# Kernel tuning notes

Hardware: AMD Instinct MI355X
Metric: run time of the kernel (lower is better)

Reference implementation:

```python
import jax, jax.numpy as jnp
import numpy as np

IN_CH = 128
OUT_CH = 32
HEADS = 4
N_NODES = 50000
N_EDGES = 500000
NEG_SLOPE = 0.01  # torch leaky_relu default


def setup_inputs() -> dict:
    key = jax.random.key(0)
    ks = jax.random.split(key, 8)
    E, D, H, C = N_EDGES, IN_CH, HEADS, OUT_CH
    receivers = jax.random.normal(ks[0], (E, D), dtype=jnp.float32)
    senders = jax.random.normal(ks[1], (E, D), dtype=jnp.float32)
    edge_attribute = jax.random.normal(ks[2], (E, D), dtype=jnp.float32)
    sender_idx = jax.random.randint(ks[3], (E,), 0, N_NODES)
    receiver_idx = jax.random.randint(ks[4], (E,), 0, N_NODES)
    # bias-free linear weights, stored as [in, heads*out] so y = x @ W
    scale = 1.0 / np.sqrt(D)
    W_src = jax.random.normal(ks[5], (D, H * C), dtype=jnp.float32) * scale
    W_tgt = jax.random.normal(ks[6], (D, H * C), dtype=jnp.float32) * scale
    W_edge = jax.random.normal(ks[7], (D, H * C), dtype=jnp.float32) * scale
    # xavier_normal_ on shape (1, H, C): std = sqrt(2/(H + C)) per torch fan calc on last two dims
    attn = jax.random.normal(jax.random.fold_in(key, 99), (1, H, C), dtype=jnp.float32) * np.sqrt(2.0 / (H + C))
    return {
        "receivers": receivers,
        "senders": senders,
        "edge_attribute": edge_attribute,
        "sender_idx": sender_idx,
        "receiver_idx": receiver_idx,
        "W_src": W_src,
        "W_tgt": W_tgt,
        "W_edge": W_edge,
        "attn": attn,
    }


def reference(receivers, senders, edge_attribute, sender_idx, receiver_idx, W_src, W_tgt, W_edge, attn):
    E = receivers.shape[0]
    H, C = HEADS, OUT_CH
    t = (receivers @ W_tgt).reshape(E, H, C)   # target projection of receiver feats
    s = (senders @ W_src).reshape(E, H, C)
    e = (edge_attribute @ W_edge).reshape(E, H, C)
    z = (jax.nn.leaky_relu(s + t + e, NEG_SLOPE) * attn).sum(-1)  # [E, H]
    # segment softmax over edges grouped by sender_idx
    zmax = jax.ops.segment_max(z, sender_idx, num_segments=N_NODES)  # [N, H]
    ez = jnp.exp(z - zmax[sender_idx])
    denom = jax.ops.segment_sum(ez, sender_idx, num_segments=N_NODES)
    a = ez / denom[sender_idx]                 # [E, H]
    m = t * a[..., None]                        # [E, H, C]
    aggr_m = jax.ops.segment_sum(m, receiver_idx, num_segments=N_NODES)  # [N, H, C]
    return aggr_m.mean(axis=1), m.mean(axis=1)  # ([N, C], [E, C])
```

## Files before the change

### kernel.cpp

```cpp
#include <hip/hip_runtime.h>
#include <hip/hip_bf16.h>

#define E_EDGES 500000
#define NN 50000

typedef unsigned short u16;
typedef __attribute__((ext_vector_type(8))) short s16x8;
typedef __attribute__((ext_vector_type(4))) float f32x4;

#define BAR() __builtin_amdgcn_s_barrier()
#define SCHED0() __builtin_amdgcn_sched_barrier(0)
#define WAITLGKM0() asm volatile("s_waitcnt lgkmcnt(0)" ::: "memory")

__device__ __forceinline__ short f2bf(float f) {
    unsigned u = __builtin_bit_cast(unsigned, f);
    u += 0x7fffu + ((u >> 16) & 1u);
    return (short)(u >> 16);
}

__device__ __forceinline__ float lrelu(float x) { return x > 0.0f ? x : 0.01f * x; }

__device__ __forceinline__ s16x8 cvt8(float4 lo, float4 hi) {
    union { s16x8 v; __hip_bfloat162 h[4]; } u;
    u.h[0] = __float22bfloat162_rn(make_float2(lo.x, lo.y));
    u.h[1] = __float22bfloat162_rn(make_float2(lo.z, lo.w));
    u.h[2] = __float22bfloat162_rn(make_float2(hi.x, hi.y));
    u.h[3] = __float22bfloat162_rn(make_float2(hi.z, hi.w));
    return u.v;
}

__global__ void kprep(const float* __restrict__ Wsrc, const float* __restrict__ Wtgt,
                      const float* __restrict__ Wedge, u16* __restrict__ WT) {
    int i = blockIdx.x * 256 + threadIdx.x;
    if (i >= 3 * 16384) return;
    int g = i >> 14, nk = i & 16383, n = nk >> 7, k = nk & 127;
    const float* W = (g == 0) ? Wsrc : (g == 1) ? Wtgt : Wedge;
    WT[i] = (u16)f2bf(W[k * 128 + n]);
}

__global__ __launch_bounds__(256, 2) void k1(
    const float* __restrict__ recv, const float* __restrict__ send,
    const float* __restrict__ eattr, const int* __restrict__ sidx,
    const u16* __restrict__ WT, const float* __restrict__ attn,
    float* __restrict__ ez, float* __restrict__ denom)
{
    __shared__ u16 ldsA[128][136];
    __shared__ u16 ldsB[128][136];
    __shared__ float smEz[4][32][4];
    const int tid = threadIdx.x;
    const int lane = tid & 63, wv = tid >> 6;
    const int l15 = lane & 15, lg = (lane >> 4) & 3;
    const int blockRow = blockIdx.x * 128;

    const float* Xg[3] = {send, recv, eattr};

    f32x4 acc[2][8];
#pragma unroll
    for (int m = 0; m < 2; ++m)
#pragma unroll
        for (int n = 0; n < 8; ++n) acc[m][n] = (f32x4){0.f, 0.f, 0.f, 0.f};

    float4 ra[2][8][2];

    auto issueA = [&](int g, int buf) {
        const float* X = Xg[g];
#pragma unroll
        for (int q = 0; q < 8; ++q) {
            int idx = tid + 256 * q;
            int row = idx >> 4, gcol = (idx & 15) * 8;
            int ge = min(blockRow + row, E_EDGES - 1);
            const float* p = X + (size_t)ge * 128 + gcol;
            ra[buf][q][0] = *(const float4*)p;
            ra[buf][q][1] = *(const float4*)(p + 4);
        }
    };

    auto commitA = [&](int buf) {
#pragma unroll
        for (int q = 0; q < 8; ++q) {
            int idx = tid + 256 * q;
            *(s16x8*)&ldsA[idx >> 4][(idx & 15) * 8] = cvt8(ra[buf][q][0], ra[buf][q][1]);
        }
    };

    auto mfma_g = [&]() {
#pragma unroll
        for (int kk = 0; kk < 4; ++kk) {
            int k0 = kk * 32 + lg * 8;
            s16x8 a0 = *(const s16x8*)&ldsA[wv * 32 + l15][k0];
            s16x8 a1 = *(const s16x8*)&ldsA[wv * 32 + 16 + l15][k0];
#pragma unroll
            for (int n = 0; n < 8; ++n) {
                s16x8 b = *(const s16x8*)&ldsB[n * 16 + l15][k0];
                acc[0][n] = __builtin_amdgcn_mfma_f32_16x16x32_bf16(a0, b, acc[0][n], 0, 0, 0);
                acc[1][n] = __builtin_amdgcn_mfma_f32_16x16x32_bf16(a1, b, acc[1][n], 0, 0, 0);
            }
        }
    };

    issueA(0, 0);
#pragma unroll
    for (int g = 0; g < 3; ++g) {
        if (g) { mfma_g(); SCHED0(); }
        BAR();
        s16x8 rb[8];
        {
            const u16* Bg = WT + g * 16384;
#pragma unroll
            for (int q = 0; q < 8; ++q) {
                int idx = tid + 256 * q;
                rb[q] = *(const s16x8*)(Bg + (idx >> 4) * 128 + (idx & 15) * 8);
            }
        }
        if (g < 2) issueA(g + 1, (g + 1) & 1);
        SCHED0();
        commitA(g & 1);
#pragma unroll
        for (int q = 0; q < 8; ++q) {
            int idx = tid + 256 * q;
            *(s16x8*)&ldsB[idx >> 4][(idx & 15) * 8] = rb[q];
        }
        SCHED0();
        WAITLGKM0();
        BAR();
    }
    mfma_g();

    float av[8];
#pragma unroll
    for (int n = 0; n < 8; ++n) av[n] = attn[n * 16 + l15];

#pragma unroll
    for (int m = 0; m < 2; ++m) {
#pragma unroll
        for (int h = 0; h < 4; ++h) {
            float part[4];
#pragma unroll
            for (int j = 0; j < 4; ++j)
                part[j] = lrelu(acc[m][2 * h][j]) * av[2 * h] +
                          lrelu(acc[m][2 * h + 1][j]) * av[2 * h + 1];
#pragma unroll
            for (int off = 1; off < 16; off <<= 1) {
#pragma unroll
                for (int j = 0; j < 4; ++j) part[j] += __shfl_xor(part[j], off, 64);
            }
            if (l15 == h) {
#pragma unroll
                for (int j = 0; j < 4; ++j)
                    smEz[wv][m * 16 + lg * 4 + j][h] = __expf(part[j]);
            }
        }
    }
    {
        int row = lane >> 1, hp = (lane & 1) * 2;
        int r = blockRow + wv * 32 + row;
        float e0 = smEz[wv][row][hp];
        float e1 = smEz[wv][row][hp + 1];
        if (r < E_EDGES) {
            *(float2*)(ez + (size_t)r * 4 + hp) = make_float2(e0, e1);
            int s = sidx[r];
            atomicAdd(&denom[(size_t)s * 4 + hp], e0);
            atomicAdd(&denom[(size_t)s * 4 + hp + 1], e1);
        }
    }
}

__global__ __launch_bounds__(256, 2) void k2(
    const float* __restrict__ recv, const int* __restrict__ ridx,
    const int* __restrict__ sidx, const u16* __restrict__ WTt,
    const float* __restrict__ ez, const float* __restrict__ denom,
    float* __restrict__ out0, float* __restrict__ out1)
{
    __shared__ u16 ldsA[128][136];
    __shared__ u16 ldsB[128][136];
    int tid = threadIdx.x;
    int lane = tid & 63, wv = tid >> 6;
    int l15 = lane & 15, lg = lane >> 4;
    int blockRow = blockIdx.x * 128;

    f32x4 acc[2][8];
#pragma unroll
    for (int m = 0; m < 2; ++m)
#pragma unroll
        for (int n = 0; n < 8; ++n) acc[m][n] = (f32x4){0.f, 0.f, 0.f, 0.f};

#pragma unroll
    for (int it = 0; it < 8; ++it) {
        int chunk = it * 256 + tid;
        int row = chunk >> 4, kc = (chunk & 15) << 3;
        int ge = min(blockRow + row, E_EDGES - 1);
        const float* p = recv + (size_t)ge * 128 + kc;
        float4 v0 = *(const float4*)p;
        float4 v1 = *(const float4*)(p + 4);
        *(s16x8*)&ldsA[row][kc] = cvt8(v0, v1);
    }
#pragma unroll
    for (int it = 0; it < 8; ++it) {
        int chunk = it * 256 + tid;
        int n = chunk >> 4, kc = (chunk & 15) << 3;
        *(s16x8*)&ldsB[n][kc] = *(const s16x8*)(WTt + n * 128 + kc);
    }
    __syncthreads();

#pragma unroll
    for (int kk = 0; kk < 4; ++kk) {
        int k0 = kk * 32 + lg * 8;
        s16x8 a0 = *(const s16x8*)&ldsA[wv * 32 + l15][k0];
        s16x8 a1 = *(const s16x8*)&ldsA[wv * 32 + 16 + l15][k0];
#pragma unroll
        for (int n = 0; n < 8; ++n) {
            s16x8 b = *(const s16x8*)&ldsB[n * 16 + l15][k0];
            acc[0][n] = __builtin_amdgcn_mfma_f32_16x16x32_bf16(a0, b, acc[0][n], 0, 0, 0);
            acc[1][n] = __builtin_amdgcn_mfma_f32_16x16x32_bf16(a1, b, acc[1][n], 0, 0, 0);
        }
    }

#pragma unroll
    for (int m = 0; m < 2; ++m) {
#pragma unroll
        for (int j = 0; j < 4; ++j) {
            int r = blockRow + wv * 32 + m * 16 + lg * 4 + j;
            if (r < E_EDGES) {
                int s = sidx[r];
                float4 ezv = *(const float4*)(ez + (size_t)r * 4);
                float4 dn = *(const float4*)(denom + (size_t)s * 4);
                float a0 = ezv.x / dn.x, a1 = ezv.y / dn.y;
                float a2 = ezv.z / dn.z, a3 = ezv.w / dn.w;
                float lo = 0.25f * (acc[m][0][j] * a0 + acc[m][2][j] * a1 +
                                    acc[m][4][j] * a2 + acc[m][6][j] * a3);
                float hi = 0.25f * (acc[m][1][j] * a0 + acc[m][3][j] * a1 +
                                    acc[m][5][j] * a2 + acc[m][7][j] * a3);
                out1[(size_t)r * 32 + l15] = lo;
                out1[(size_t)r * 32 + 16 + l15] = hi;
                int rv = ridx[r];
                atomicAdd(&out0[(size_t)rv * 32 + l15], lo);
                atomicAdd(&out0[(size_t)rv * 32 + 16 + l15], hi);
            }
        }
    }
}

extern "C" void kernel_launch(void* const* d_in, const int* in_sizes, int n_in,
                              void* d_out, int out_size, void* d_ws, size_t ws_size,
                              hipStream_t stream) {
    const float* recv  = (const float*)d_in[0];
    const float* send  = (const float*)d_in[1];
    const float* eattr = (const float*)d_in[2];
    const int*   sidx  = (const int*)d_in[3];
    const int*   ridx  = (const int*)d_in[4];
    const float* Wsrc  = (const float*)d_in[5];
    const float* Wtgt  = (const float*)d_in[6];
    const float* Wedge = (const float*)d_in[7];
    const float* attn  = (const float*)d_in[8];

    char* ws = (char*)d_ws;
    u16*   WT    = (u16*)ws;
    float* ez    = (float*)(ws + 131072);
    float* denom = (float*)(ws + 131072 + 8000000);

    float* out0 = (float*)d_out;
    float* out1 = out0 + (size_t)NN * 32;

    hipMemsetAsync(denom, 0, (size_t)NN * 4 * sizeof(float), stream);
    hipMemsetAsync(out0, 0, (size_t)NN * 32 * sizeof(float), stream);

    kprep<<<192, 256, 0, stream>>>(Wsrc, Wtgt, Wedge, WT);

    int nb = (E_EDGES + 127) / 128;
    k1<<<nb, 256, 0, stream>>>(recv, send, eattr, sidx, WT, attn, ez, denom);
    k2<<<nb, 256, 0, stream>>>(recv, ridx, sidx, WT + 16384, ez, denom, out0, out1);
}
```

Before: 305.2 us.

## Make k1 persistent over tile ranges with cross-tile activation prefetch

k1 now launches a fixed grid of 512 blocks, each processing a contiguous range of 7–8 row tiles (3907 tiles total), instead of one block per tile. The activation load for the next projection, and for the first projection of the next tile, is issued before the current MFMA work, so global loads overlap compute across tile boundaries. The input order is changed to send/eattr/recv, and attn is loaded once per block. This trades a single register buffer and a grid sized to the CU count for less launch and tail overhead, but the weight tiles are still reloaded into LDS for every projection.

```diff
diff --git a/kernel.cpp b/kernel.cpp
--- a/kernel.cpp
+++ b/kernel.cpp
@@ -50,36 +50,38 @@
     const int tid = threadIdx.x;
     const int lane = tid & 63, wv = tid >> 6;
     const int l15 = lane & 15, lg = (lane >> 4) & 3;
-    const int blockRow = blockIdx.x * 128;
-
-    const float* Xg[3] = {send, recv, eattr};
+
+    const int b = blockIdx.x;
+    const int start = b * 7 + min(b, 323);
+    const int end = start + 7 + (b < 323 ? 1 : 0);
+
+    const float* Xg[3] = {send, eattr, recv};
+    const int bgoff[3] = {0, 2 * 16384, 1 * 16384};
+
+    float av[8];
+#pragma unroll
+    for (int n = 0; n < 8; ++n) av[n] = attn[n * 16 + l15];
 
     f32x4 acc[2][8];
-#pragma unroll
-    for (int m = 0; m < 2; ++m)
-#pragma unroll
-        for (int n = 0; n < 8; ++n) acc[m][n] = (f32x4){0.f, 0.f, 0.f, 0.f};
-
-    float4 ra[2][8][2];
-
-    auto issueA = [&](int g, int buf) {
-        const float* X = Xg[g];
+    float4 ra[8][2];
+
+    auto issueA = [&](const float* X, int tileRow) {
 #pragma unroll
         for (int q = 0; q < 8; ++q) {
             int idx = tid + 256 * q;
             int row = idx >> 4, gcol = (idx & 15) * 8;
-            int ge = min(blockRow + row, E_EDGES - 1);
+            int ge = min(tileRow + row, E_EDGES - 1);
             const float* p = X + (size_t)ge * 128 + gcol;
-            ra[buf][q][0] = *(const float4*)p;
-            ra[buf][q][1] = *(const float4*)(p + 4);
+            ra[q][0] = *(const float4*)p;
+            ra[q][1] = *(const float4*)(p + 4);
         }
     };
 
-    auto commitA = [&](int buf) {
+    auto commitA = [&]() {
 #pragma unroll
         for (int q = 0; q < 8; ++q) {
             int idx = tid + 256 * q;
-            *(s16x8*)&ldsA[idx >> 4][(idx & 15) * 8] = cvt8(ra[buf][q][0], ra[buf][q][1]);
+            *(s16x8*)&ldsA[idx >> 4][(idx & 15) * 8] = cvt8(ra[q][0], ra[q][1]);
         }
     };
 
@@ -91,76 +93,81 @@
             s16x8 a1 = *(const s16x8*)&ldsA[wv * 32 + 16 + l15][k0];
 #pragma unroll
             for (int n = 0; n < 8; ++n) {
-                s16x8 b = *(const s16x8*)&ldsB[n * 16 + l15][k0];
-                acc[0][n] = __builtin_amdgcn_mfma_f32_16x16x32_bf16(a0, b, acc[0][n], 0, 0, 0);
-                acc[1][n] = __builtin_amdgcn_mfma_f32_16x16x32_bf16(a1, b, acc[1][n], 0, 0, 0);
+                s16x8 bfr = *(const s16x8*)&ldsB[n * 16 + l15][k0];
+                acc[0][n] = __builtin_amdgcn_mfma_f32_16x16x32_bf16(a0, bfr, acc[0][n], 0, 0, 0);
+                acc[1][n] = __builtin_amdgcn_mfma_f32_16x16x32_bf16(a1, bfr, acc[1][n], 0, 0, 0);
             }
         }
     };
 
-    issueA(0, 0);
-#pragma unroll
-    for (int g = 0; g < 3; ++g) {
-        if (g) { mfma_g(); SCHED0(); }
-        BAR();
-        s16x8 rb[8];
-        {
-            const u16* Bg = WT + g * 16384;
+    issueA(Xg[0], start * 128);
+
+    for (int t = start; t < end; ++t) {
+        const int row0 = t * 128;
+#pragma unroll
+        for (int m = 0; m < 2; ++m)
+#pragma unroll
+            for (int n = 0; n < 8; ++n) acc[m][n] = (f32x4){0.f, 0.f, 0.f, 0.f};
+
+#pragma unroll
+        for (int g = 0; g < 3; ++g) {
+            BAR();
+            s16x8 rb[8];
+            {
+                const u16* Bg = WT + bgoff[g];
+#pragma unroll
+                for (int q = 0; q < 8; ++q) {
+                    int idx = tid + 256 * q;
+                    rb[q] = *(const s16x8*)(Bg + (idx >> 4) * 128 + (idx & 15) * 8);
+                }
+            }
+            commitA();
+            if (g < 2) issueA(Xg[g + 1], row0);
+            else if (t + 1 < end) issueA(Xg[0], row0 + 128);
+            SCHED0();
 #pragma unroll
             for (int q = 0; q < 8; ++q) {
                 int idx = tid + 256 * q;
-                rb[q] = *(const s16x8*)(Bg + (idx >> 4) * 128 + (idx & 15) * 8);
-            }
-        }
-        if (g < 2) issueA(g + 1, (g + 1) & 1);
-        SCHED0();
-        commitA(g & 1);
-#pragma unroll
-        for (int q = 0; q < 8; ++q) {
-            int idx = tid + 256 * q;
-            *(s16x8*)&ldsB[idx >> 4][(idx & 15) * 8] = rb[q];
-        }
-        SCHED0();
-        WAITLGKM0();
-        BAR();
-    }
-    mfma_g();
-
-    float av[8];
-#pragma unroll
-    for (int n = 0; n < 8; ++n) av[n] = attn[n * 16 + l15];
-
-#pragma unroll
-    for (int m = 0; m < 2; ++m) {
-#pragma unroll
-        for (int h = 0; h < 4; ++h) {
-            float part[4];
-#pragma unroll
-            for (int j = 0; j < 4; ++j)
-                part[j] = lrelu(acc[m][2 * h][j]) * av[2 * h] +
-                          lrelu(acc[m][2 * h + 1][j]) * av[2 * h + 1];
-#pragma unroll
-            for (int off = 1; off < 16; off <<= 1) {
-#pragma unroll
-                for (int j = 0; j < 4; ++j) part[j] += __shfl_xor(part[j], off, 64);
-            }
-            if (l15 == h) {
+                *(s16x8*)&ldsB[idx >> 4][(idx & 15) * 8] = rb[q];
+            }
+            SCHED0();
+            WAITLGKM0();
+            BAR();
+            mfma_g();
+        }
+
+#pragma unroll
+        for (int m = 0; m < 2; ++m) {
+#pragma unroll
+            for (int h = 0; h < 4; ++h) {
+                float part[4];
 #pragma unroll
                 for (int j = 0; j < 4; ++j)
-                    smEz[wv][m * 16 + lg * 4 + j][h] = __expf(part[j]);
-            }
-        }
-    }
-    {
-        int row = lane >> 1, hp = (lane & 1) * 2;
-        int r = blockRow + wv * 32 + row;
-        float e0 = smEz[wv][row][hp];
-        float e1 = smEz[wv][row][hp + 1];
-        if (r < E_EDGES) {
-            *(float2*)(ez + (size_t)r * 4 + hp) = make_float2(e0, e1);
-            int s = sidx[r];
-            atomicAdd(&denom[(size_t)s * 4 + hp], e0);
-            atomicAdd(&denom[(size_t)s * 4 + hp + 1], e1);
+                    part[j] = lrelu(acc[m][2 * h][j]) * av[2 * h] +
+                              lrelu(acc[m][2 * h + 1][j]) * av[2 * h + 1];
+#pragma unroll
+                for (int off = 1; off < 16; off <<= 1) {
+#pragma unroll
+                    for (int j = 0; j < 4; ++j) part[j] += __shfl_xor(part[j], off, 64);
+                }
+                if (l15 == h) {
+#pragma unroll
+                    for (int j = 0; j < 4; ++j)
+                        smEz[wv][m * 16 + lg * 4 + j][h] = __expf(part[j]);
+                }
+            }
+        }
+        {
+            int row = lane >> 1, hp = (lane & 1) * 2;
+            int r = row0 + wv * 32 + row;
+            float e0 = smEz[wv][row][hp];
+            float e1 = smEz[wv][row][hp + 1];
+            if (r < E_EDGES) {
+                *(float2*)(ez + (size_t)r * 4 + hp) = make_float2(e0, e1);
+                int s = sidx[r];
+                atomicAdd(&denom[(size_t)s * 4 + hp], e0);
+                atomicAdd(&denom[(size_t)s * 4 + hp + 1], e1);
+            }
         }
     }
 }
@@ -266,7 +273,7 @@
 
     kprep<<<192, 256, 0, stream>>>(Wsrc, Wtgt, Wedge, WT);
 
-    int nb = (E_EDGES + 127) / 128;
-    k1<<<nb, 256, 0, stream>>>(recv, send, eattr, sidx, WT, attn, ez, denom);
-    k2<<<nb, 256, 0, stream>>>(recv, ridx, sidx, WT + 16384, ez, denom, out0, out1);
-}
+    k1<<<512, 256, 0, stream>>>(recv, send, eattr, sidx, WT, attn, ez, denom);
+    int nb2 = (E_EDGES + 127) / 128;
+    k2<<<nb2, 256, 0, stream>>>(recv, ridx, sidx, WT + 16384, ez, denom, out0, out1);
+}
```

Result: slower. 322.5 us (+5.7%).
